# Kernel optimization log

Hardware: AMD Instinct MI355X
Metric: run time of the kernel (lower is better)

The kernel has to match this reference:

```python
import jax, jax.numpy as jnp
import numpy as np

D = 128      # cfg.gt.dim_hidden
L = 4        # cfg.gt.layers


def _seg_mean(x, idx, n):
    s = jax.ops.segment_sum(x, idx, num_segments=n)
    c = jax.ops.segment_sum(jnp.ones((idx.shape[0], 1), x.dtype), idx, num_segments=n)
    return s / jnp.maximum(c, 1.0)


def setup_inputs() -> dict:
    key = jax.random.key(0)
    ks = jax.random.split(key, 12)
    N, E, M, EC, P = 50000, 400000, 200000, 800000, 2000
    x = jax.random.normal(ks[0], (N, D), dtype=jnp.float32)
    edge_attr = jax.random.normal(ks[1], (E, D), dtype=jnp.float32)
    subgraphs_nodes_mapper = jax.random.randint(ks[2], (M,), 0, N)
    subgraphs_edges_mapper = jax.random.randint(ks[3], (EC,), 0, E)
    combined_subgraphs = jax.random.randint(ks[4], (2, EC), 0, M)
    subgraphs_batch = jnp.sort(jax.random.randint(ks[5], (M,), 0, P))
    sc = 1.0 / np.sqrt(D)
    W_gnn = jax.random.normal(ks[6], (L, D, D), dtype=jnp.float32) * sc
    b_gnn = jnp.zeros((L, D), dtype=jnp.float32)
    eps = jnp.zeros((L,), dtype=jnp.float32)
    W_u = jax.random.normal(ks[7], (L - 1, D, D), dtype=jnp.float32) * sc
    b_u = jnp.zeros((L - 1, D), dtype=jnp.float32)
    return {
        "x": x, "edge_attr": edge_attr,
        "subgraphs_nodes_mapper": subgraphs_nodes_mapper,
        "subgraphs_edges_mapper": subgraphs_edges_mapper,
        "combined_subgraphs": combined_subgraphs,
        "subgraphs_batch": subgraphs_batch,
        "num_patches": P,
        "W_gnn": W_gnn, "b_gnn": b_gnn, "eps": eps,
        "W_u": W_u, "b_u": b_u,
    }


def reference(x, edge_attr, subgraphs_nodes_mapper, subgraphs_edges_mapper,
              combined_subgraphs, subgraphs_batch, num_patches,
              W_gnn, b_gnn, eps, W_u, b_u):
    N = x.shape[0]
    M = subgraphs_nodes_mapper.shape[0]
    h = x[subgraphs_nodes_mapper]                 # [M, D] gather into subgraph copies
    e = edge_attr[subgraphs_edges_mapper]         # [EC, D]
    src, dst = combined_subgraphs[0], combined_subgraphs[1]
    for i in range(L):
        if i > 0:
            sub = _seg_mean(h, subgraphs_batch, num_patches)[subgraphs_batch]
            h = h + jax.nn.relu(sub @ W_u[i - 1] + b_u[i - 1])
            h = _seg_mean(h, subgraphs_nodes_mapper, N)[subgraphs_nodes_mapper]
        # GINEConv: W((1+eps)*h + sum_j relu(h_j + e_ij)) + b
        msg = jax.nn.relu(h[src] + e)             # [EC, D]
        agg = jax.ops.segment_sum(msg, dst, num_segments=M)
        h = ((1.0 + eps[i]) * h + agg) @ W_gnn[i] + b_gnn[i]
    # mean pooling per patch (cfg.gt.pooling = 'mean')
    subgraph_x = _seg_mean(h, subgraphs_batch, num_patches)  # [P, D]
    return subgraph_x
```

## Files before the change

### kernel.cpp

```cpp
#include <hip/hip_runtime.h>
#include <hip/hip_bf16.h>

#define D 128
#define DV 32

typedef float4 f4;
typedef unsigned short ushort_t;
typedef unsigned int uint_t;
typedef __attribute__((ext_vector_type(8))) short short8;
typedef __attribute__((ext_vector_type(8))) unsigned short ushort8;
typedef __attribute__((ext_vector_type(4))) float f32x4;
typedef __attribute__((ext_vector_type(2))) float f32x2;

__device__ __forceinline__ void f4add(f4& a, const f4& b) {
    a.x += b.x; a.y += b.y; a.z += b.z; a.w += b.w;
}
__device__ __forceinline__ float b2f(ushort_t u) {
    union { unsigned int i; float f; } v; v.i = ((unsigned int)u) << 16; return v.f;
}
__device__ __forceinline__ ushort_t f2b(float f) {
    __hip_bfloat16 b = __float2bfloat16(f);
    return *reinterpret_cast<ushort_t*>(&b);
}
__device__ __forceinline__ f4 fp8x4_to_f4(uint_t v) {
    f32x2 lo = __builtin_amdgcn_cvt_pk_f32_fp8((int)v, false);
    f32x2 hi = __builtin_amdgcn_cvt_pk_f32_fp8((int)v, true);
    return make_float4(lo[0], lo[1], hi[0], hi[1]);
}
__device__ __forceinline__ uint_t f4_to_fp8x4(f4 v) {
    int r = 0;
    r = __builtin_amdgcn_cvt_pk_fp8_f32(v.x, v.y, r, false);
    r = __builtin_amdgcn_cvt_pk_fp8_f32(v.z, v.w, r, true);
    return (uint_t)r;
}

__global__ void k_histm(const int* __restrict__ dst, const int* __restrict__ nm,
                        const int* __restrict__ batch, int* __restrict__ ecnt,
                        int* __restrict__ ncnt, int* __restrict__ pcnt, int EC, int M) {
    int c = blockIdx.x * 256 + threadIdx.x;
    if (c < EC) atomicAdd(&ecnt[dst[c]], 1);
    if (c < M) { atomicAdd(&ncnt[nm[c]], 1); atomicAdd(&pcnt[batch[c]], 1); }
}

__global__ __launch_bounds__(256) void k_scan1m(const int* __restrict__ inE, int* __restrict__ outE, int nbe, int nE,
                                                const int* __restrict__ inN, int* __restrict__ outN, int nbn, int nN,
                                                const int* __restrict__ inP, int* __restrict__ outP, int nbp, int nP,
                                                int* __restrict__ bsum) {
    __shared__ int ts[256];
    int b = blockIdx.x, t = threadIdx.x;
    const int* in; int* out; int* bs; int lb, n;
    if (b < nbe)            { in = inE; out = outE; bs = bsum;       lb = b;             n = nE; }
    else if (b < nbe + nbn) { in = inN; out = outN; bs = bsum + 256; lb = b - nbe;       n = nN; }
    else                    { in = inP; out = outP; bs = bsum + 512; lb = b - nbe - nbn; n = nP; }
    int base = lb * 1024 + t * 4;
    int v0 = base + 0 < n ? in[base + 0] : 0;
    int v1 = base + 1 < n ? in[base + 1] : 0;
    int v2 = base + 2 < n ? in[base + 2] : 0;
    int v3 = base + 3 < n ? in[base + 3] : 0;
    int tot = v0 + v1 + v2 + v3;
    ts[t] = tot; __syncthreads();
    for (int off = 1; off < 256; off <<= 1) {
        int x = (t >= off) ? ts[t - off] : 0; __syncthreads();
        ts[t] += x; __syncthreads();
    }
    int ex = ts[t] - tot;
    if (base + 0 < n) out[base + 0] = ex;
    if (base + 1 < n) out[base + 1] = ex + v0;
    if (base + 2 < n) out[base + 2] = ex + v0 + v1;
    if (base + 3 < n) out[base + 3] = ex + v0 + v1 + v2;
    if (t == 255) bs[lb] = ts[255];
}

__global__ __launch_bounds__(256) void k_scan2m(int* __restrict__ bsum, int nbe, int nbn, int nbp) {
    __shared__ int ts[256];
    int b = blockIdx.x, t = threadIdx.x;
    int* a; int n;
    if (b == 0)      { a = bsum;       n = nbe; }
    else if (b == 1) { a = bsum + 256; n = nbn; }
    else             { a = bsum + 512; n = nbp; }
    int base = t * 4;
    int v0 = base + 0 < n ? a[base + 0] : 0;
    int v1 = base + 1 < n ? a[base + 1] : 0;
    int v2 = base + 2 < n ? a[base + 2] : 0;
    int v3 = base + 3 < n ? a[base + 3] : 0;
    int tot = v0 + v1 + v2 + v3;
    ts[t] = tot; __syncthreads();
    for (int off = 1; off < 256; off <<= 1) {
        int x = (t >= off) ? ts[t - off] : 0; __syncthreads();
        ts[t] += x; __syncthreads();
    }
    int ex = ts[t] - tot;
    if (base + 0 < n) a[base + 0] = ex;
    if (base + 1 < n) a[base + 1] = ex + v0;
    if (base + 2 < n) a[base + 2] = ex + v0 + v1;
    if (base + 3 < n) a[base + 3] = ex + v0 + v1 + v2;
}

__global__ void k_scan3m(int* __restrict__ outE, int* __restrict__ outN, int* __restrict__ outP,
                         const int* __restrict__ bsum, int nE, int nN, int nP) {
    int i = blockIdx.x * 256 + threadIdx.x;
    if (i < nE) { outE[i] += bsum[i >> 10]; return; }
    i -= nE;
    if (i < nN) { outN[i] += bsum[256 + (i >> 10)]; return; }
    i -= nN;
    if (i < nP) { outP[i] += bsum[512 + (i >> 10)]; }
}

__global__ void k_scatterm(const int* __restrict__ dst, const int* __restrict__ src,
                           const int* __restrict__ em, const int* __restrict__ nm,
                           const int* __restrict__ batch,
                           int* __restrict__ ecur, int2* __restrict__ se,
                           int* __restrict__ ncur, int* __restrict__ mlist, int* __restrict__ pb,
                           int EC, int M) {
    int c = blockIdx.x * 256 + threadIdx.x;
    if (c < EC) {
        int p = atomicAdd(&ecur[dst[c]], 1);
        se[p] = make_int2(nm[src[c]], em[c]);
    }
    if (c < M) {
        int p = atomicAdd(&ncur[nm[c]], 1);
        mlist[p] = c;
        pb[p] = batch[c];
    }
}

__global__ void k_convm(const float* __restrict__ ea, uint_t* __restrict__ eab4, int EA4,
                        const float* __restrict__ x, ushort_t* __restrict__ xb, int NX8,
                        const float* __restrict__ Wg, ushort_t* __restrict__ Wtb, int NW) {
    int i = blockIdx.x * 256 + threadIdx.x;
    if (i < EA4) {
        f4 v = *((const f4*)ea + (size_t)i);
        eab4[i] = f4_to_fp8x4(v);
        return;
    }
    i -= EA4;
    if (i < NX8) {
        const f4* p = (const f4*)x + (size_t)i * 2;
        f4 v0 = p[0], v1 = p[1];
        ushort4 o0, o1;
        o0.x = f2b(v0.x); o0.y = f2b(v0.y); o0.z = f2b(v0.z); o0.w = f2b(v0.w);
        o1.x = f2b(v1.x); o1.y = f2b(v1.y); o1.z = f2b(v1.z); o1.w = f2b(v1.w);
        *(ushort4*)(xb + (size_t)i * 8) = o0;
        *(ushort4*)(xb + (size_t)i * 8 + 4) = o1;
        return;
    }
    i -= NX8;
    if (i < NW) {
        int l = i >> 14, rem = i & 16383;
        int col = rem >> 7, k = rem & 127;
        Wtb[(size_t)l * 16384 + col * 128 + k] = f2b(Wg[(size_t)l * 16384 + k * 128 + col]);
    }
}

__global__ __launch_bounds__(256) void k_edge(const ushort_t* __restrict__ hnb,
                                              const uint_t* __restrict__ eab4,
                                              const int* __restrict__ nm, const int2* __restrict__ se,
                                              const int* __restrict__ eend, const int* __restrict__ ecnt,
                                              ushort_t* __restrict__ aggb,
                                              const float* __restrict__ eps, int layer, int M) {
    int idx = blockIdx.x * 256 + threadIdx.x;
    int d = idx >> 4, j = idx & 15;
    if (d >= M) return;
    float s = 1.0f + eps[layer];
    ushort8 hb = *(const ushort8*)(hnb + (size_t)nm[d] * D + j * 8);
    float acc[8];
#pragma unroll
    for (int q = 0; q < 8; q++) acc[q] = b2f(hb[q]) * s;
    int kn = eend[d], k0 = kn - ecnt[d];
    int k = k0;
    for (; k + 2 <= kn; k += 2) {
        int2 se0 = se[k], se1 = se[k + 1];
        uint2 p0 = *(const uint2*)(eab4 + (size_t)se0.y * 32 + j * 2);
        uint2 p1 = *(const uint2*)(eab4 + (size_t)se1.y * 32 + j * 2);
        ushort8 h0 = *(const ushort8*)(hnb + (size_t)se0.x * D + j * 8);
        ushort8 h1 = *(const ushort8*)(hnb + (size_t)se1.x * D + j * 8);
        f4 e0a = fp8x4_to_f4(p0.x), e0b = fp8x4_to_f4(p0.y);
        f4 e1a = fp8x4_to_f4(p1.x), e1b = fp8x4_to_f4(p1.y);
        acc[0] += fmaxf(b2f(h0[0]) + e0a.x, 0.f) + fmaxf(b2f(h1[0]) + e1a.x, 0.f);
        acc[1] += fmaxf(b2f(h0[1]) + e0a.y, 0.f) + fmaxf(b2f(h1[1]) + e1a.y, 0.f);
        acc[2] += fmaxf(b2f(h0[2]) + e0a.z, 0.f) + fmaxf(b2f(h1[2]) + e1a.z, 0.f);
        acc[3] += fmaxf(b2f(h0[3]) + e0a.w, 0.f) + fmaxf(b2f(h1[3]) + e1a.w, 0.f);
        acc[4] += fmaxf(b2f(h0[4]) + e0b.x, 0.f) + fmaxf(b2f(h1[4]) + e1b.x, 0.f);
        acc[5] += fmaxf(b2f(h0[5]) + e0b.y, 0.f) + fmaxf(b2f(h1[5]) + e1b.y, 0.f);
        acc[6] += fmaxf(b2f(h0[6]) + e0b.z, 0.f) + fmaxf(b2f(h1[6]) + e1b.z, 0.f);
        acc[7] += fmaxf(b2f(h0[7]) + e0b.w, 0.f) + fmaxf(b2f(h1[7]) + e1b.w, 0.f);
    }
    if (k < kn) {
        int2 se0 = se[k];
        uint2 p0 = *(const uint2*)(eab4 + (size_t)se0.y * 32 + j * 2);
        ushort8 h0 = *(const ushort8*)(hnb + (size_t)se0.x * D + j * 8);
        f4 e0a = fp8x4_to_f4(p0.x), e0b = fp8x4_to_f4(p0.y);
        acc[0] += fmaxf(b2f(h0[0]) + e0a.x, 0.f);
        acc[1] += fmaxf(b2f(h0[1]) + e0a.y, 0.f);
        acc[2] += fmaxf(b2f(h0[2]) + e0a.z, 0.f);
        acc[3] += fmaxf(b2f(h0[3]) + e0a.w, 0.f);
        acc[4] += fmaxf(b2f(h0[4]) + e0b.x, 0.f);
        acc[5] += fmaxf(b2f(h0[5]) + e0b.y, 0.f);
        acc[6] += fmaxf(b2f(h0[6]) + e0b.z, 0.f);
        acc[7] += fmaxf(b2f(h0[7]) + e0b.w, 0.f);
    }
    ushort8 o;
#pragma unroll
    for (int q = 0; q < 8; q++) o[q] = f2b(acc[q]);
    *(ushort8*)(aggb + (size_t)d * D + j * 8) = o;
}

__global__ __launch_bounds__(256) void k_patch_tf(const ushort_t* __restrict__ aggb,
                                                  const int* __restrict__ pstart, const int* __restrict__ pcnt,
                                                  const float* __restrict__ Wg, const float* __restrict__ bg,
                                                  const float* __restrict__ Wu, const float* __restrict__ bu,
                                                  float* __restrict__ pmu, float* __restrict__ outv, int layer) {
    __shared__ f4 red[256];
    __shared__ float row[D];
    __shared__ float gp[256];
    int p = blockIdx.x;
    int t = threadIdx.x, j = t & 31, r = t >> 5;
    int s0 = pstart[p], c = pcnt[p];
    f4 acc = make_float4(0.f, 0.f, 0.f, 0.f);
    for (int k = r; k < c; k += 8) {
        ushort4 ab = *(const ushort4*)(aggb + (size_t)(s0 + k) * D + j * 4);
        acc.x += b2f(ab.x); acc.y += b2f(ab.y); acc.z += b2f(ab.z); acc.w += b2f(ab.w);
    }
    red[t] = acc; __syncthreads();
    for (int step = 4; step >= 1; step >>= 1) {
        if (r < step) f4add(red[t], red[t + 32 * step]);
        __syncthreads();
    }
    if (r == 0) {
        f4 a = red[j];
        float inv = 1.0f / fmaxf((float)c, 1.0f);
        a.x *= inv; a.y *= inv; a.z *= inv; a.w *= inv;
        *(f4*)&row[j * 4] = a;
    }
    __syncthreads();
    int col = t & 127, half = t >> 7;
    {
        const float* W = Wg + (size_t)layer * D * D;
        float g = 0.f;
        int kb = half * 64;
#pragma unroll 8
        for (int k = 0; k < 64; k++) g += row[kb + k] * W[(kb + k) * D + col];
        gp[t] = g;
    }
    __syncthreads();
    if (layer == 3) {
        if (t < D) outv[(size_t)p * D + t] = gp[t] + gp[t + 128] + bg[layer * D + t];
        return;
    }
    __shared__ float mid[D];
    if (t < D) mid[t] = gp[t] + gp[t + 128] + bg[layer * D + t];
    __syncthreads();
    {
        const float* W2 = Wu + (size_t)layer * D * D;
        float g = 0.f;
        int kb = half * 64;
#pragma unroll 8
        for (int k = 0; k < 64; k++) g += mid[kb + k] * W2[(kb + k) * D + col];
        gp[t] = g;
    }
    __syncthreads();
    if (t < D) pmu[(size_t)p * D + t] = fmaxf(gp[t] + gp[t + 128] + bu[layer * D + t], 0.f);
}

__global__ __launch_bounds__(256) void k_nagg(const ushort_t* __restrict__ aggb,
                                              const float* __restrict__ pmu,
                                              const int* __restrict__ pb, const int* __restrict__ mlist,
                                              const int* __restrict__ nend, const int* __restrict__ ncnt,
                                              ushort_t* __restrict__ naggb, ushort_t* __restrict__ pmusum,
                                              int N) {
    int idx = blockIdx.x * 256 + threadIdx.x;
    int n = idx >> 4, j = idx & 15;
    if (n >= N) return;
    int kn = nend[n], c = ncnt[n], s0 = kn - c;
    float sa[8] = {0.f, 0.f, 0.f, 0.f, 0.f, 0.f, 0.f, 0.f};
    float sp[8] = {0.f, 0.f, 0.f, 0.f, 0.f, 0.f, 0.f, 0.f};
    for (int k = 0; k < c; k++) {
        int m = mlist[s0 + k];
        int pbv = pb[s0 + k];
        ushort8 ab = *(const ushort8*)(aggb + (size_t)m * D + j * 8);
        const f4* pp = (const f4*)(pmu + (size_t)pbv * D) + j * 2;
        f4 pv0 = pp[0], pv1 = pp[1];
#pragma unroll
        for (int q = 0; q < 8; q++) sa[q] += b2f(ab[q]);
        sp[0] += pv0.x; sp[1] += pv0.y; sp[2] += pv0.z; sp[3] += pv0.w;
        sp[4] += pv1.x; sp[5] += pv1.y; sp[6] += pv1.z; sp[7] += pv1.w;
    }
    float inv = 1.0f / fmaxf((float)c, 1.0f);
    ushort8 o, q8;
#pragma unroll
    for (int q = 0; q < 8; q++) { o[q] = f2b(sa[q] * inv); q8[q] = f2b(sp[q] * inv); }
    *(ushort8*)(naggb + (size_t)n * D + j * 8) = o;
    *(ushort8*)(pmusum + (size_t)n * D + j * 8) = q8;
}

__global__ __launch_bounds__(256) void k_nup(const ushort_t* __restrict__ naggb,
                                             const ushort_t* __restrict__ Wtb,
                                             const float* __restrict__ bg,
                                             const ushort_t* __restrict__ pmusum,
                                             ushort_t* __restrict__ hnb, int N, int layer) {
    __shared__ ushort_t Wl[128 * 136];
    const ushort_t* W = Wtb + (size_t)layer * D * D;
    int t = threadIdx.x;
#pragma unroll
    for (int i = 0; i < 8; i++) {
        int cid = t + i * 256;
        int col = cid >> 4, kc = (cid & 15) * 8;
        *(short8*)&Wl[col * 136 + kc] = *(const short8*)(W + col * 128 + kc);
    }
    __syncthreads();
    int w = t >> 6, lane = t & 63;
    int r16 = lane & 15, kg = lane >> 4;
    int rowbase = blockIdx.x * 64 + w * 16;
    size_t arow = (size_t)min(rowbase + r16, N - 1) * D;
    short8 a0 = *(const short8*)(naggb + arow + 0 + kg * 8);
    short8 a1 = *(const short8*)(naggb + arow + 32 + kg * 8);
    short8 a2 = *(const short8*)(naggb + arow + 64 + kg * 8);
    short8 a3 = *(const short8*)(naggb + arow + 96 + kg * 8);
#pragma unroll
    for (int c = 0; c < 8; c++) {
        const ushort_t* wp = &Wl[(c * 16 + r16) * 136 + kg * 8];
        short8 b0 = *(const short8*)(wp + 0);
        short8 b1 = *(const short8*)(wp + 32);
        short8 b2 = *(const short8*)(wp + 64);
        short8 b3 = *(const short8*)(wp + 96);
        f32x4 acc = (f32x4){0.f, 0.f, 0.f, 0.f};
        acc = __builtin_amdgcn_mfma_f32_16x16x32_bf16(a0, b0, acc, 0, 0, 0);
        acc = __builtin_amdgcn_mfma_f32_16x16x32_bf16(a1, b1, acc, 0, 0, 0);
        acc = __builtin_amdgcn_mfma_f32_16x16x32_bf16(a2, b2, acc, 0, 0, 0);
        acc = __builtin_amdgcn_mfma_f32_16x16x32_bf16(a3, b3, acc, 0, 0, 0);
        int gcol = c * 16 + r16;
        float bias = bg[layer * D + gcol];
#pragma unroll
        for (int q = 0; q < 4; q++) {
            int grow = rowbase + kg * 4 + q;
            if (grow < N)
                hnb[(size_t)grow * D + gcol] =
                    f2b(acc[q] + bias + b2f(pmusum[(size_t)grow * D + gcol]));
        }
    }
}

extern "C" void kernel_launch(void* const* d_in, const int* in_sizes, int n_in,
                              void* d_out, int out_size, void* d_ws, size_t ws_size,
                              hipStream_t stream) {
    const float* x    = (const float*)d_in[0];
    const float* ea   = (const float*)d_in[1];
    const int* nm     = (const int*)d_in[2];
    const int* em     = (const int*)d_in[3];
    const int* cs     = (const int*)d_in[4];
    const int* batch  = (const int*)d_in[5];
    const float* Wg   = (const float*)d_in[7];
    const float* bg   = (const float*)d_in[8];
    const float* eps  = (const float*)d_in[9];
    const float* Wu   = (const float*)d_in[10];
    const float* bu   = (const float*)d_in[11];
    float* out = (float*)d_out;

    int N  = in_sizes[0] / D;
    int E  = in_sizes[1] / D;
    int M  = in_sizes[2];
    int EC = in_sizes[3];
    int P  = out_size / D;
    const int* src = cs;
    const int* dst = cs + EC;

    char* base = (char*)d_ws;
    size_t off = 0;
    auto carve = [&](size_t bytes) { void* p = base + off; off += (bytes + 255) & ~(size_t)255; return p; };
    ushort_t* aggb   = (ushort_t*)carve((size_t)M * D * 2);
    uint_t*   eab4   = (uint_t*)carve((size_t)E * D);
    ushort_t* xb     = (ushort_t*)carve((size_t)N * D * 2);
    ushort_t* Wtb    = (ushort_t*)carve((size_t)4 * D * D * 2);
    ushort_t* hnb    = (ushort_t*)carve((size_t)N * D * 2);
    ushort_t* naggb  = (ushort_t*)carve((size_t)N * D * 2);
    ushort_t* pmusum = (ushort_t*)carve((size_t)N * D * 2);
    float*    pmu    = (float*)carve((size_t)P * D * 4);
    int* cntblk = (int*)carve((size_t)(M + N + P) * 4);
    int* ecnt = cntblk, *ncnt = cntblk + M, *pcnt = cntblk + M + N;
    int* ecur   = (int*)carve((size_t)M * 4);
    int* ncur   = (int*)carve((size_t)N * 4);
    int2* se    = (int2*)carve((size_t)EC * 8);
    int* mlist  = (int*)carve((size_t)M * 4);
    int* pb     = (int*)carve((size_t)M * 4);
    int* pstart = (int*)carve((size_t)P * 4);
    int* bsum   = (int*)carve(768 * 4);
    if (ws_size < off) return;

    hipMemsetAsync(cntblk, 0, (size_t)(M + N + P) * sizeof(int), stream);
    int mxEM = EC > M ? EC : M;
    k_histm<<<(mxEM + 255) / 256, 256, 0, stream>>>(dst, nm, batch, ecnt, ncnt, pcnt, EC, M);

    int nbe = (M + 1023) / 1024, nbn = (N + 1023) / 1024, nbp = (P + 1023) / 1024;
    k_scan1m<<<nbe + nbn + nbp, 256, 0, stream>>>(ecnt, ecur, nbe, M,
                                                  ncnt, ncur, nbn, N,
                                                  pcnt, pstart, nbp, P, bsum);
    k_scan2m<<<3, 256, 0, stream>>>(bsum, nbe, nbn, nbp);
    k_scan3m<<<(M + N + P + 255) / 256, 256, 0, stream>>>(ecur, ncur, pstart, bsum, M, N, P);

    k_scatterm<<<(mxEM + 255) / 256, 256, 0, stream>>>(dst, src, em, nm, batch,
                                                       ecur, se, ncur, mlist, pb, EC, M);
    int EA4 = E * D / 4, NX8 = N * D / 8, NW = 4 * D * D;
    k_convm<<<(EA4 + NX8 + NW + 255) / 256, 256, 0, stream>>>(ea, eab4, EA4, x, xb, NX8, Wg, Wtb, NW);

    int mb = (M * 16 + 255) / 256;
    int nb = (N * 16 + 255) / 256;
    for (int i = 0; i < 4; i++) {
        const ushort_t* hnp = (i == 0) ? xb : hnb;
        if (i > 0) {
            k_nagg<<<nb, 256, 0, stream>>>(aggb, pmu, pb, mlist,
                                           ncur, ncnt, naggb, pmusum, N);
            k_nup<<<(N + 63) / 64, 256, 0, stream>>>(naggb, Wtb, bg, pmusum, hnb, N, i - 1);
        }
        k_edge<<<mb, 256, 0, stream>>>(hnp, eab4, nm, se, ecur, ecnt, aggb, eps, i, M);
        k_patch_tf<<<P, 256, 0, stream>>>(aggb, pstart, pcnt, Wg, bg, Wu, bu, pmu, out, i);
    }
}
```

Baseline: 607.3 us.

## Split patch transform into mean kernel plus MFMA GEMM, unroll edge loop by four

The per-patch kernel used to do the mean and two 128x128 matvecs in scalar fp32, reading the weights once per patch. It is now split into a patch-mean kernel that writes bf16 means and a batched MFMA kernel that handles 64 patches per block, using transposed bf16 copies of both weight sets staged in shared memory. The patch MLP output pmu is now stored in bf16, which halves its reads in k_nagg, and the edge aggregation loop is unrolled from 2 to 4 edges for more memory-level parallelism. The cost is an extra launch per layer and reduced precision in the patch path.

```diff
diff --git a/kernel.cpp b/kernel.cpp
--- a/kernel.cpp
+++ b/kernel.cpp
@@ -126,7 +126,8 @@
 
 __global__ void k_convm(const float* __restrict__ ea, uint_t* __restrict__ eab4, int EA4,
                         const float* __restrict__ x, ushort_t* __restrict__ xb, int NX8,
-                        const float* __restrict__ Wg, ushort_t* __restrict__ Wtb, int NW) {
+                        const float* __restrict__ Wg, ushort_t* __restrict__ Wtb, int NW,
+                        const float* __restrict__ Wu, ushort_t* __restrict__ Wub, int NW2) {
     int i = blockIdx.x * 256 + threadIdx.x;
     if (i < EA4) {
         f4 v = *((const f4*)ea + (size_t)i);
@@ -149,6 +150,13 @@
         int l = i >> 14, rem = i & 16383;
         int col = rem >> 7, k = rem & 127;
         Wtb[(size_t)l * 16384 + col * 128 + k] = f2b(Wg[(size_t)l * 16384 + k * 128 + col]);
+        return;
+    }
+    i -= NW;
+    if (i < NW2) {
+        int l = i >> 14, rem = i & 16383;
+        int col = rem >> 7, k = rem & 127;
+        Wub[(size_t)l * 16384 + col * 128 + k] = f2b(Wu[(size_t)l * 16384 + k * 128 + col]);
     }
 }
 
@@ -168,24 +176,38 @@
     for (int q = 0; q < 8; q++) acc[q] = b2f(hb[q]) * s;
     int kn = eend[d], k0 = kn - ecnt[d];
     int k = k0;
-    for (; k + 2 <= kn; k += 2) {
-        int2 se0 = se[k], se1 = se[k + 1];
+    for (; k + 4 <= kn; k += 4) {
+        int2 se0 = se[k], se1 = se[k + 1], se2 = se[k + 2], se3 = se[k + 3];
         uint2 p0 = *(const uint2*)(eab4 + (size_t)se0.y * 32 + j * 2);
         uint2 p1 = *(const uint2*)(eab4 + (size_t)se1.y * 32 + j * 2);
+        uint2 p2 = *(const uint2*)(eab4 + (size_t)se2.y * 32 + j * 2);
+        uint2 p3 = *(const uint2*)(eab4 + (size_t)se3.y * 32 + j * 2);
         ushort8 h0 = *(const ushort8*)(hnb + (size_t)se0.x * D + j * 8);
         ushort8 h1 = *(const ushort8*)(hnb + (size_t)se1.x * D + j * 8);
+        ushort8 h2 = *(const ushort8*)(hnb + (size_t)se2.x * D + j * 8);
+        ushort8 h3 = *(const ushort8*)(hnb + (size_t)se3.x * D + j * 8);
         f4 e0a = fp8x4_to_f4(p0.x), e0b = fp8x4_to_f4(p0.y);
         f4 e1a = fp8x4_to_f4(p1.x), e1b = fp8x4_to_f4(p1.y);
-        acc[0] += fmaxf(b2f(h0[0]) + e0a.x, 0.f) + fmaxf(b2f(h1[0]) + e1a.x, 0.f);
-        acc[1] += fmaxf(b2f(h0[1]) + e0a.y, 0.f) + fmaxf(b2f(h1[1]) + e1a.y, 0.f);
-        acc[2] += fmaxf(b2f(h0[2]) + e0a.z, 0.f) + fmaxf(b2f(h1[2]) + e1a.z, 0.f);
-        acc[3] += fmaxf(b2f(h0[3]) + e0a.w, 0.f) + fmaxf(b2f(h1[3]) + e1a.w, 0.f);
-        acc[4] += fmaxf(b2f(h0[4]) + e0b.x, 0.f) + fmaxf(b2f(h1[4]) + e1b.x, 0.f);
-        acc[5] += fmaxf(b2f(h0[5]) + e0b.y, 0.f) + fmaxf(b2f(h1[5]) + e1b.y, 0.f);
-        acc[6] += fmaxf(b2f(h0[6]) + e0b.z, 0.f) + fmaxf(b2f(h1[6]) + e1b.z, 0.f);
-        acc[7] += fmaxf(b2f(h0[7]) + e0b.w, 0.f) + fmaxf(b2f(h1[7]) + e1b.w, 0.f);
-    }
-    if (k < kn) {
+        f4 e2a = fp8x4_to_f4(p2.x), e2b = fp8x4_to_f4(p2.y);
+        f4 e3a = fp8x4_to_f4(p3.x), e3b = fp8x4_to_f4(p3.y);
+        acc[0] += (fmaxf(b2f(h0[0]) + e0a.x, 0.f) + fmaxf(b2f(h1[0]) + e1a.x, 0.f))
+                + (fmaxf(b2f(h2[0]) + e2a.x, 0.f) + fmaxf(b2f(h3[0]) + e3a.x, 0.f));
+        acc[1] += (fmaxf(b2f(h0[1]) + e0a.y, 0.f) + fmaxf(b2f(h1[1]) + e1a.y, 0.f))
+                + (fmaxf(b2f(h2[1]) + e2a.y, 0.f) + fmaxf(b2f(h3[1]) + e3a.y, 0.f));
+        acc[2] += (fmaxf(b2f(h0[2]) + e0a.z, 0.f) + fmaxf(b2f(h1[2]) + e1a.z, 0.f))
+                + (fmaxf(b2f(h2[2]) + e2a.z, 0.f) + fmaxf(b2f(h3[2]) + e3a.z, 0.f));
+        acc[3] += (fmaxf(b2f(h0[3]) + e0a.w, 0.f) + fmaxf(b2f(h1[3]) + e1a.w, 0.f))
+                + (fmaxf(b2f(h2[3]) + e2a.w, 0.f) + fmaxf(b2f(h3[3]) + e3a.w, 0.f));
+        acc[4] += (fmaxf(b2f(h0[4]) + e0b.x, 0.f) + fmaxf(b2f(h1[4]) + e1b.x, 0.f))
+                + (fmaxf(b2f(h2[4]) + e2b.x, 0.f) + fmaxf(b2f(h3[4]) + e3b.x, 0.f));
+        acc[5] += (fmaxf(b2f(h0[5]) + e0b.y, 0.f) + fmaxf(b2f(h1[5]) + e1b.y, 0.f))
+                + (fmaxf(b2f(h2[5]) + e2b.y, 0.f) + fmaxf(b2f(h3[5]) + e3b.y, 0.f));
+        acc[6] += (fmaxf(b2f(h0[6]) + e0b.z, 0.f) + fmaxf(b2f(h1[6]) + e1b.z, 0.f))
+                + (fmaxf(b2f(h2[6]) + e2b.z, 0.f) + fmaxf(b2f(h3[6]) + e3b.z, 0.f));
+        acc[7] += (fmaxf(b2f(h0[7]) + e0b.w, 0.f) + fmaxf(b2f(h1[7]) + e1b.w, 0.f))
+                + (fmaxf(b2f(h2[7]) + e2b.w, 0.f) + fmaxf(b2f(h3[7]) + e3b.w, 0.f));
+    }
+    for (; k < kn; k++) {
         int2 se0 = se[k];
         uint2 p0 = *(const uint2*)(eab4 + (size_t)se0.y * 32 + j * 2);
         ushort8 h0 = *(const ushort8*)(hnb + (size_t)se0.x * D + j * 8);
@@ -205,14 +227,10 @@
     *(ushort8*)(aggb + (size_t)d * D + j * 8) = o;
 }
 
-__global__ __launch_bounds__(256) void k_patch_tf(const ushort_t* __restrict__ aggb,
-                                                  const int* __restrict__ pstart, const int* __restrict__ pcnt,
-                                                  const float* __restrict__ Wg, const float* __restrict__ bg,
-                                                  const float* __restrict__ Wu, const float* __restrict__ bu,
-                                                  float* __restrict__ pmu, float* __restrict__ outv, int layer) {
+__global__ __launch_bounds__(256) void k_patch_agg(const ushort_t* __restrict__ aggb,
+                                                   const int* __restrict__ pstart, const int* __restrict__ pcnt,
+                                                   ushort_t* __restrict__ pmean) {
     __shared__ f4 red[256];
-    __shared__ float row[D];
-    __shared__ float gp[256];
     int p = blockIdx.x;
     int t = threadIdx.x, j = t & 31, r = t >> 5;
     int s0 = pstart[p], c = pcnt[p];
@@ -229,41 +247,102 @@
     if (r == 0) {
         f4 a = red[j];
         float inv = 1.0f / fmaxf((float)c, 1.0f);
-        a.x *= inv; a.y *= inv; a.z *= inv; a.w *= inv;
-        *(f4*)&row[j * 4] = a;
+        ushort4 o;
+        o.x = f2b(a.x * inv); o.y = f2b(a.y * inv); o.z = f2b(a.z * inv); o.w = f2b(a.w * inv);
+        *(ushort4*)(pmean + (size_t)p * D + j * 4) = o;
+    }
+}
+
+__global__ __launch_bounds__(256) void k_ptf_mfma(const ushort_t* __restrict__ pmean,
+                                                  const ushort_t* __restrict__ Wtb, const float* __restrict__ bg,
+                                                  const ushort_t* __restrict__ Wub, const float* __restrict__ bu,
+                                                  ushort_t* __restrict__ pmu, float* __restrict__ outv,
+                                                  int P_, int layer) {
+    __shared__ ushort_t Wl[128 * 136];
+    __shared__ ushort_t midl[64 * 136];
+    int t = threadIdx.x;
+    const ushort_t* W = Wtb + (size_t)layer * D * D;
+#pragma unroll
+    for (int i = 0; i < 8; i++) {
+        int cid = t + i * 256;
+        int col = cid >> 4, kc = (cid & 15) * 8;
+        *(short8*)&Wl[col * 136 + kc] = *(const short8*)(W + col * 128 + kc);
     }
     __syncthreads();
-    int col = t & 127, half = t >> 7;
-    {
-        const float* W = Wg + (size_t)layer * D * D;
-        float g = 0.f;
-        int kb = half * 64;
-#pragma unroll 8
-        for (int k = 0; k < 64; k++) g += row[kb + k] * W[(kb + k) * D + col];
-        gp[t] = g;
-    }
+    int w = t >> 6, lane = t & 63;
+    int r16 = lane & 15, kg = lane >> 4;
+    int rowbase = blockIdx.x * 64 + w * 16;
+    size_t arow = (size_t)min(rowbase + r16, P_ - 1) * D;
+    short8 a0 = *(const short8*)(pmean + arow + 0 + kg * 8);
+    short8 a1 = *(const short8*)(pmean + arow + 32 + kg * 8);
+    short8 a2 = *(const short8*)(pmean + arow + 64 + kg * 8);
+    short8 a3 = *(const short8*)(pmean + arow + 96 + kg * 8);
+#pragma unroll
+    for (int c = 0; c < 8; c++) {
+        const ushort_t* wp = &Wl[(c * 16 + r16) * 136 + kg * 8];
+        short8 b0 = *(const short8*)(wp + 0);
+        short8 b1 = *(const short8*)(wp + 32);
+        short8 b2 = *(const short8*)(wp + 64);
+        short8 b3 = *(const short8*)(wp + 96);
+        f32x4 acc = (f32x4){0.f, 0.f, 0.f, 0.f};
+        acc = __builtin_amdgcn_mfma_f32_16x16x32_bf16(a0, b0, acc, 0, 0, 0);
+        acc = __builtin_amdgcn_mfma_f32_16x16x32_bf16(a1, b1, acc, 0, 0, 0);
+        acc = __builtin_amdgcn_mfma_f32_16x16x32_bf16(a2, b2, acc, 0, 0, 0);
+        acc = __builtin_amdgcn_mfma_f32_16x16x32_bf16(a3, b3, acc, 0, 0, 0);
+        int gcol = c * 16 + r16;
+        float bias = bg[layer * D + gcol];
+#pragma unroll
+        for (int q = 0; q < 4; q++) {
+            int lrow = w * 16 + kg * 4 + q;
+            float v = acc[q] + bias;
+            if (layer == 3) {
+                int grow = rowbase - w * 16 + lrow;
+                if (grow < P_) outv[(size_t)grow * D + gcol] = v;
+            } else {
+                midl[lrow * 136 + gcol] = f2b(v);
+            }
+        }
+    }
+    if (layer == 3) return;
     __syncthreads();
-    if (layer == 3) {
-        if (t < D) outv[(size_t)p * D + t] = gp[t] + gp[t + 128] + bg[layer * D + t];
-        return;
-    }
-    __shared__ float mid[D];
-    if (t < D) mid[t] = gp[t] + gp[t + 128] + bg[layer * D + t];
+    const ushort_t* W2 = Wub + (size_t)layer * D * D;
+#pragma unroll
+    for (int i = 0; i < 8; i++) {
+        int cid = t + i * 256;
+        int col = cid >> 4, kc = (cid & 15) * 8;
+        *(short8*)&Wl[col * 136 + kc] = *(const short8*)(W2 + col * 128 + kc);
+    }
     __syncthreads();
-    {
-        const float* W2 = Wu + (size_t)layer * D * D;
-        float g = 0.f;
-        int kb = half * 64;
-#pragma unroll 8
-        for (int k = 0; k < 64; k++) g += mid[kb + k] * W2[(kb + k) * D + col];
-        gp[t] = g;
-    }
-    __syncthreads();
-    if (t < D) pmu[(size_t)p * D + t] = fmaxf(gp[t] + gp[t + 128] + bu[layer * D + t], 0.f);
+    const ushort_t* mp = &midl[(w * 16 + r16) * 136 + kg * 8];
+    short8 m0 = *(const short8*)(mp + 0);
+    short8 m1 = *(const short8*)(mp + 32);
+    short8 m2 = *(const short8*)(mp + 64);
+    short8 m3 = *(const short8*)(mp + 96);
+#pragma unroll
+    for (int c = 0; c < 8; c++) {
+        const ushort_t* wp = &Wl[(c * 16 + r16) * 136 + kg * 8];
+        short8 b0 = *(const short8*)(wp + 0);
+        short8 b1 = *(const short8*)(wp + 32);
+        short8 b2 = *(const short8*)(wp + 64);
+        short8 b3 = *(const short8*)(wp + 96);
+        f32x4 acc = (f32x4){0.f, 0.f, 0.f, 0.f};
+        acc = __builtin_amdgcn_mfma_f32_16x16x32_bf16(m0, b0, acc, 0, 0, 0);
+        acc = __builtin_amdgcn_mfma_f32_16x16x32_bf16(m1, b1, acc, 0, 0, 0);
+        acc = __builtin_amdgcn_mfma_f32_16x16x32_bf16(m2, b2, acc, 0, 0, 0);
+        acc = __builtin_amdgcn_mfma_f32_16x16x32_bf16(m3, b3, acc, 0, 0, 0);
+        int gcol = c * 16 + r16;
+        float bias = bu[layer * D + gcol];
+#pragma unroll
+        for (int q = 0; q < 4; q++) {
+            int grow = blockIdx.x * 64 + w * 16 + kg * 4 + q;
+            if (grow < P_)
+                pmu[(size_t)grow * D + gcol] = f2b(fmaxf(acc[q] + bias, 0.f));
+        }
+    }
 }
 
 __global__ __launch_bounds__(256) void k_nagg(const ushort_t* __restrict__ aggb,
-                                              const float* __restrict__ pmu,
+                                              const ushort_t* __restrict__ pmu,
                                               const int* __restrict__ pb, const int* __restrict__ mlist,
                                               const int* __restrict__ nend, const int* __restrict__ ncnt,
                                               ushort_t* __restrict__ naggb, ushort_t* __restrict__ pmusum,
@@ -278,12 +357,9 @@
         int m = mlist[s0 + k];
         int pbv = pb[s0 + k];
         ushort8 ab = *(const ushort8*)(aggb + (size_t)m * D + j * 8);
-        const f4* pp = (const f4*)(pmu + (size_t)pbv * D) + j * 2;
-        f4 pv0 = pp[0], pv1 = pp[1];
-#pragma unroll
-        for (int q = 0; q < 8; q++) sa[q] += b2f(ab[q]);
-        sp[0] += pv0.x; sp[1] += pv0.y; sp[2] += pv0.z; sp[3] += pv0.w;
-        sp[4] += pv1.x; sp[5] += pv1.y; sp[6] += pv1.z; sp[7] += pv1.w;
+        ushort8 pv = *(const ushort8*)(pmu + (size_t)pbv * D + j * 8);
+#pragma unroll
+        for (int q = 0; q < 8; q++) { sa[q] += b2f(ab[q]); sp[q] += b2f(pv[q]); }
     }
     float inv = 1.0f / fmaxf((float)c, 1.0f);
     ushort8 o, q8;
@@ -371,10 +447,12 @@
     uint_t*   eab4   = (uint_t*)carve((size_t)E * D);
     ushort_t* xb     = (ushort_t*)carve((size_t)N * D * 2);
     ushort_t* Wtb    = (ushort_t*)carve((size_t)4 * D * D * 2);
+    ushort_t* Wub    = (ushort_t*)carve((size_t)3 * D * D * 2);
     ushort_t* hnb    = (ushort_t*)carve((size_t)N * D * 2);
     ushort_t* naggb  = (ushort_t*)carve((size_t)N * D * 2);
     ushort_t* pmusum = (ushort_t*)carve((size_t)N * D * 2);
-    float*    pmu    = (float*)carve((size_t)P * D * 4);
+    ushort_t* pmean  = (ushort_t*)carve((size_t)P * D * 2);
+    ushort_t* pmu    = (ushort_t*)carve((size_t)P * D * 2);
     int* cntblk = (int*)carve((size_t)(M + N + P) * 4);
     int* ecnt = cntblk, *ncnt = cntblk + M, *pcnt = cntblk + M + N;
     int* ecur   = (int*)carve((size_t)M * 4);
@@ -399,11 +477,13 @@
 
     k_scatterm<<<(mxEM + 255) / 256, 256, 0, stream>>>(dst, src, em, nm, batch,
                                                        ecur, se, ncur, mlist, pb, EC, M);
-    int EA4 = E * D / 4, NX8 = N * D / 8, NW = 4 * D * D;
-    k_convm<<<(EA4 + NX8 + NW + 255) / 256, 256, 0, stream>>>(ea, eab4, EA4, x, xb, NX8, Wg, Wtb, NW);
+    int EA4 = E * D / 4, NX8 = N * D / 8, NW = 4 * D * D, NW2 = 3 * D * D;
+    k_convm<<<(EA4 + NX8 + NW + NW2 + 255) / 256, 256, 0, stream>>>(ea, eab4, EA4, x, xb, NX8,
+                                                                    Wg, Wtb, NW, Wu, Wub, NW2);
 
     int mb = (M * 16 + 255) / 256;
     int nb = (N * 16 + 255) / 256;
+    int pblk = (P + 63) / 64;
     for (int i = 0; i < 4; i++) {
         const ushort_t* hnp = (i == 0) ? xb : hnb;
         if (i > 0) {
@@ -412,6 +492,7 @@
             k_nup<<<(N + 63) / 64, 256, 0, stream>>>(naggb, Wtb, bg, pmusum, hnb, N, i - 1);
         }
         k_edge<<<mb, 256, 0, stream>>>(hnp, eab4, nm, se, ecur, ecnt, aggb, eps, i, M);
-        k_patch_tf<<<P, 256, 0, stream>>>(aggb, pstart, pcnt, Wg, bg, Wu, bu, pmu, out, i);
-    }
-}
+        k_patch_agg<<<P, 256, 0, stream>>>(aggb, pstart, pcnt, pmean);
+        k_ptf_mfma<<<pblk, 256, 0, stream>>>(pmean, Wtb, bg, Wub, bu, pmu, out, P, i);
+    }
+}
```

After: 618.0 us. Within noise of the previous version (+1.8%).
